# Performance work log

Hardware: AMD Instinct MI355X
Metric: run time of the kernel (lower is better)

## Reference

```python
import jax, jax.numpy as jnp
import numpy as np

B = 16          # graphs per batch
NPER = 1024     # nodes per graph (max_nodes for to_dense_batch)
N = B * NPER    # total nodes
D = 128         # hidden_dim
H = 8           # nhead
E = 524288      # total edges (avg degree 32)
DFF = 512       # dim_feedforward
LN_EPS = 1e-5


def setup_inputs() -> dict:
    key = jax.random.key(0)
    ks = jax.random.split(key, 26)
    w = lambda k, shape, s=0.05: (jax.random.normal(k, shape, jnp.float32) * s)
    h = jax.random.normal(ks[0], (N, D), jnp.float32)
    edge_index = jax.random.randint(ks[1], (2, E), 0, N, jnp.int32)
    edge_attr = jax.random.normal(ks[2], (E, D), jnp.float32)
    # nodes are in a random 'original' order; sort_idx sorts them by graph id
    sort_idx = jax.random.permutation(ks[3], N).astype(jnp.int32)
    unsort_idx = jnp.argsort(sort_idx).astype(jnp.int32)
    sorted_batch = jnp.repeat(jnp.arange(B, dtype=jnp.int32), NPER)
    batch = jnp.zeros((N,), jnp.int32).at[sort_idx].set(sorted_batch)
    return {
        "h": h, "edge_attr": edge_attr,
        # GINEConv: edge linear + 2-layer gin MLP
        "edge_w": w(ks[4], (D, D)), "edge_b": w(ks[5], (D,)),
        "gin_w1": w(ks[6], (D, D)), "gin_b1": w(ks[7], (D,)),
        "gin_w2": w(ks[8], (D, D)), "gin_b2": w(ks[9], (D,)),
        # MultiheadAttention packed qkv + out proj
        "in_proj_w": w(ks[10], (3 * D, D)), "in_proj_b": w(ks[11], (3 * D,)),
        "out_w": w(ks[12], (D, D)), "out_b": w(ks[13], (D,)),
        # FFN
        "ffn_w1": w(ks[14], (DFF, D)), "ffn_b1": w(ks[15], (DFF,)),
        "ffn_w2": w(ks[16], (D, DFF)), "ffn_b2": w(ks[17], (D,)),
        # LayerNorms
        "ln1_w": jnp.ones((D,)), "ln1_b": jnp.zeros((D,)),
        "ln2_w": jnp.ones((D,)), "ln2_b": jnp.zeros((D,)),
        "ln3_w": jnp.ones((D,)), "ln3_b": jnp.zeros((D,)),
        "edge_index": edge_index, "batch": batch,
        "sort_idx": sort_idx, "unsort_idx": unsort_idx,
    }


def _layer_norm(x, w, b):
    mu = x.mean(-1, keepdims=True)
    var = ((x - mu) ** 2).mean(-1, keepdims=True)
    return (x - mu) * jax.lax.rsqrt(var + LN_EPS) * w + b


def reference(h, edge_attr, edge_w, edge_b, gin_w1, gin_b1, gin_w2, gin_b2,
              in_proj_w, in_proj_b, out_w, out_b,
              ffn_w1, ffn_b1, ffn_w2, ffn_b2,
              ln1_w, ln1_b, ln2_w, ln2_b, ln3_w, ln3_b,
              edge_index, batch, sort_idx, unsort_idx):
    residual = h
    # ---- local branch: GINEConv (eps=0) -----------------------------------
    src, dst = edge_index[0], edge_index[1]
    e = edge_attr @ edge_w.T + edge_b                      # [E, D]
    msg = jax.nn.relu(h[src] + e)                          # gather + fuse
    agg = jax.ops.segment_sum(msg, dst, num_segments=N)    # scatter-add
    x = h + agg                                            # (1+eps)*x_i + aggr
    h_local = jax.nn.relu(x @ gin_w1.T + gin_b1) @ gin_w2.T + gin_b2
    # ---- global branch: sort -> dense batch -> MHA -> unsort --------------
    hs = h[sort_idx]
    bs = batch[sort_idx]
    counts = jax.ops.segment_sum(jnp.ones((N,), jnp.int32), bs, num_segments=B)
    ptr = jnp.concatenate([jnp.zeros((1,), jnp.int32),
                           jnp.cumsum(counts)[:-1].astype(jnp.int32)])
    pos = jnp.arange(N, dtype=jnp.int32) - ptr[bs]         # slot within graph
    dense = jnp.zeros((B, NPER, D), h.dtype).at[bs, pos].set(hs)
    mask = jnp.zeros((B, NPER), bool).at[bs, pos].set(True)
    qkv = dense @ in_proj_w.T + in_proj_b                  # [B, NPER, 3D]
    q, k, v = jnp.split(qkv, 3, axis=-1)
    hd = D // H
    q = q.reshape(B, NPER, H, hd)
    k = k.reshape(B, NPER, H, hd)
    v = v.reshape(B, NPER, H, hd)
    scores = jnp.einsum('bqhd,bkhd->bhqk', q, k) / np.float32(np.sqrt(hd))
    scores = jnp.where(mask[:, None, None, :], scores, jnp.float32(-1e9))
    attn = jax.nn.softmax(scores, axis=-1)
    ao = jnp.einsum('bhqk,bkhd->bqhd', attn, v).reshape(B, NPER, D)
    ao = ao @ out_w.T + out_b
    h_attn = ao[bs, pos][unsort_idx]                       # dense->flat->unsort
    # ---- residual + norms + FFN -------------------------------------------
    h1 = _layer_norm(residual + h_local, ln1_w, ln1_b)
    h2 = _layer_norm(h1 + h_attn, ln2_w, ln2_b)
    ffn = jax.nn.gelu(h2 @ ffn_w1.T + ffn_b1, approximate=False) @ ffn_w2.T + ffn_b2
    return _layer_norm(h2 + ffn, ln3_w, ln3_b)
```

## Files before the change

### kernel.cpp

```cpp
#include <hip/hip_runtime.h>
#include <cmath>

typedef __attribute__((ext_vector_type(4))) float  f32x4;
typedef __attribute__((ext_vector_type(16))) float f32x16;
typedef __attribute__((ext_vector_type(2))) float  f32x2;
typedef __attribute__((ext_vector_type(8))) short  s16x8;
typedef __attribute__((ext_vector_type(4))) short  s16x4;
typedef __attribute__((ext_vector_type(2))) short  s16x2;
typedef __attribute__((ext_vector_type(4))) int    i32x4;

#define DEV __device__ __forceinline__

DEV float bf2f(short s) {
    unsigned int u = ((unsigned int)(unsigned short)s) << 16;
    return __builtin_bit_cast(float, u);
}
DEV short f2bs(float f) {
    unsigned int x = __builtin_bit_cast(unsigned int, f);
    x += 0x7fffu + ((x >> 16) & 1u);
    return (short)(x >> 16);
}
DEV s16x8 ld8(const void* p, size_t off, int m) {
    s16x8 r;
    if (m) {
        const float* f = (const float*)p + off;
        f32x4 a = *(const f32x4*)f, b = *(const f32x4*)(f + 4);
#pragma unroll
        for (int j = 0; j < 4; ++j) { r[j] = f2bs(a[j]); r[4 + j] = f2bs(b[j]); }
    } else {
        r = *(const s16x8*)((const short*)p + off);
    }
    return r;
}
DEV float ldf(const void* p, size_t off, int m) {
    return m ? ((const float*)p)[off] : bf2f(((const short*)p)[off]);
}

__global__ void probe_kernel(const unsigned* __restrict__ w1, int* __restrict__ flag)
{
    if (threadIdx.x == 0 && blockIdx.x == 0)
        flag[0] = (w1[0] == 0x3F800000u) ? 1 : 0;
}

__global__ void hist_kernel(const int* __restrict__ edst, int* __restrict__ cnt)
{
    int e = blockIdx.x * 256 + threadIdx.x;
    atomicAdd(&cnt[edst[e]], 1);
}

__global__ __launch_bounds__(1024)
void scan_kernel(const int* __restrict__ cnt, int* __restrict__ cursor)
{
    __shared__ int s[1024];
    int t = threadIdx.x;
    int v[16];
    int sum = 0;
#pragma unroll
    for (int j = 0; j < 16; ++j) { v[j] = cnt[t * 16 + j]; sum += v[j]; }
    s[t] = sum;
    __syncthreads();
    for (int off = 1; off < 1024; off <<= 1) {
        int x = (t >= off) ? s[t - off] : 0;
        __syncthreads();
        s[t] += x;
        __syncthreads();
    }
    int running = s[t] - sum;
#pragma unroll
    for (int j = 0; j < 16; ++j) { cursor[t * 16 + j] = running; running += v[j]; }
}

__global__ void scatter_kernel(const int* __restrict__ esrc, const int* __restrict__ edst,
                               int* __restrict__ cursor, int* __restrict__ sEid,
                               int* __restrict__ sDst, int* __restrict__ sSrc)
{
    int e = blockIdx.x * 256 + threadIdx.x;
    int d = edst[e];
    int pos = atomicAdd(&cursor[d], 1);
    sEid[pos] = e;
    sDst[pos] = d;
    sSrc[pos] = esrc[e];
}

__global__ __launch_bounds__(256, 2)
void edge_agg_kernel(const void* __restrict__ EA, const void* __restrict__ EW,
                     const void* __restrict__ EB, const void* __restrict__ H,
                     const int* __restrict__ sEid, const int* __restrict__ sDst,
                     const int* __restrict__ sSrc,
                     float* __restrict__ agg, const int* __restrict__ modep)
{
    const int m = *modep;
    __shared__ short Ws[128][136];
    int tid = threadIdx.x;
#pragma unroll
    for (int i = 0; i < 8; ++i) {
        int id = i * 256 + tid;
        int r = id >> 4, c = (id & 15) << 3;
        *(s16x8*)&Ws[r][c] = ld8(EW, (size_t)r * 128 + c, m);
    }
    __syncthreads();

    int wave = tid >> 6, lane = tid & 63;
    int lq = lane & 15, quad = lane >> 4;
    int ebw = blockIdx.x * 256 + wave * 64;

    float ebias[8];
#pragma unroll
    for (int nt = 0; nt < 8; ++nt) ebias[nt] = ldf(EB, nt * 16 + lq, m);

    float run[8] = {};
    int run_d = -1;

    for (int t = 0; t < 4; ++t) {
        int arow = ebw + ((lq >> 2) << 4) + t * 4 + (lq & 3);
        int aeid = sEid[arow];
        s16x8 af[4];
        const size_t abase = (size_t)aeid * 128 + quad * 8;
#pragma unroll
        for (int kb = 0; kb < 4; ++kb)
            af[kb] = ld8(EA, abase + kb * 32, m);

        f32x4 acc[8] = {};
#pragma unroll
        for (int kb = 0; kb < 4; ++kb) {
#pragma unroll
            for (int nt = 0; nt < 8; ++nt) {
                s16x8 bfr = *(const s16x8*)&Ws[nt * 16 + lq][kb * 32 + quad * 8];
                acc[nt] = __builtin_amdgcn_mfma_f32_16x16x32_bf16(af[kb], bfr, acc[nt], 0, 0, 0);
            }
        }

        int pbase = ebw + quad * 16 + t * 4;
        i32x4 dv = *(const i32x4*)&sDst[pbase];
        i32x4 sv = *(const i32x4*)&sSrc[pbase];
#pragma unroll
        for (int r = 0; r < 4; ++r) {
            int d = dv[r];
            if (d != run_d) {
                if (run_d >= 0) {
#pragma unroll
                    for (int nt = 0; nt < 8; ++nt)
                        atomicAdd(&agg[(size_t)run_d * 128 + nt * 16 + lq], run[nt]);
                }
                run_d = d;
#pragma unroll
                for (int nt = 0; nt < 8; ++nt) run[nt] = 0.f;
            }
#pragma unroll
            for (int nt = 0; nt < 8; ++nt) {
                float v = acc[nt][r] + ebias[nt] + ldf(H, (size_t)sv[r] * 128 + nt * 16 + lq, m);
                run[nt] += fmaxf(v, 0.f);
            }
        }
    }
    if (run_d >= 0) {
#pragma unroll
        for (int nt = 0; nt < 8; ++nt)
            atomicAdd(&agg[(size_t)run_d * 128 + nt * 16 + lq], run[nt]);
    }
}

__global__ void xadd_kernel(const void* __restrict__ H, const float* __restrict__ agg,
                            short* __restrict__ X, const int* __restrict__ modep)
{
    const int m = *modep;
    int i = (blockIdx.x * 256 + threadIdx.x) * 4;
    float hv[4];
    if (m) { f32x4 t = *(const f32x4*)((const float*)H + i);
#pragma unroll
             for (int j = 0; j < 4; ++j) hv[j] = t[j]; }
    else   { s16x4 t = *(const s16x4*)((const short*)H + i);
#pragma unroll
             for (int j = 0; j < 4; ++j) hv[j] = bf2f(t[j]); }
    f32x4 av = *(const f32x4*)&agg[i];
    s16x4 o;
#pragma unroll
    for (int j = 0; j < 4; ++j) o[j] = f2bs(hv[j] + av[j]);
    *(s16x4*)&X[i] = o;
}

template<int KTOT, int ACT, bool GATHER, bool XIN>
__global__ __launch_bounds__(256, 2)
void gemm_bt(const void* __restrict__ X, const int* __restrict__ ridx,
             const void* __restrict__ W, const void* __restrict__ B,
             short* __restrict__ Y, int N, const int* __restrict__ modep)
{
    const int m = *modep;
    const int xm = XIN ? m : 0;
    __shared__ short As[64][136];
    __shared__ short Wsh[64][136];
    int tid = threadIdx.x;
    int wave = tid >> 6, lane = tid & 63;
    int lq = lane & 15, quad = lane >> 4;
    int mbase = blockIdx.x * 64, nbase = blockIdx.y * 64;

    f32x4 acc[4] = {};
    for (int kc = 0; kc < KTOT / 128; ++kc) {
#pragma unroll
        for (int i = 0; i < 4; ++i) {
            int id = i * 256 + tid;
            int r = id >> 4, c = (id & 15) << 3;
            int srow = GATHER ? ridx[mbase + r] : (mbase + r);
            *(s16x8*)&As[r][c]  = ld8(X, (size_t)srow * KTOT + kc * 128 + c, xm);
            *(s16x8*)&Wsh[r][c] = ld8(W, (size_t)(nbase + r) * KTOT + kc * 128 + c, m);
        }
        __syncthreads();
        s16x8 af[4];
#pragma unroll
        for (int kb = 0; kb < 4; ++kb)
            af[kb] = *(const s16x8*)&As[wave * 16 + lq][kb * 32 + quad * 8];
#pragma unroll
        for (int kb = 0; kb < 4; ++kb) {
#pragma unroll
            for (int nt = 0; nt < 4; ++nt) {
                s16x8 bfr = *(const s16x8*)&Wsh[nt * 16 + lq][kb * 32 + quad * 8];
                acc[nt] = __builtin_amdgcn_mfma_f32_16x16x32_bf16(af[kb], bfr, acc[nt], 0, 0, 0);
            }
        }
        __syncthreads();
    }
#pragma unroll
    for (int nt = 0; nt < 4; ++nt) {
        int col = nbase + nt * 16 + lq;
        float bias = ldf(B, col, m);
#pragma unroll
        for (int r = 0; r < 4; ++r) {
            int row = mbase + wave * 16 + quad * 4 + r;
            float v = acc[nt][r] + bias;
            if (ACT == 1) v = fmaxf(v, 0.f);
            if (ACT == 2) v = 0.5f * v * (1.f + erff(v * 0.70710678118f));
            Y[(size_t)row * N + col] = f2bs(v);
        }
    }
}

__global__ __launch_bounds__(256, 2)
void attn_kernel(const short* __restrict__ QKV, short* __restrict__ AO)
{
    __shared__ __align__(16) short Ks[2048][8];
    __shared__ __align__(16) short Vt[16][1032];
    int bid = blockIdx.x;
    int qc = bid & 3, bh = bid >> 2;
    int b = bh >> 3, hh = bh & 7;
    int t = threadIdx.x;
    const short* base = QKV + (size_t)b * 1024 * 384 + hh * 16;

#pragma unroll
    for (int i = 0; i < 8; ++i) {
        int idx = i * 256 + t;
        int c = idx >> 10, kv = idx & 1023;
        const short* r = base + (size_t)kv * 384;
        *(s16x8*)&Ks[c * 1024 + kv][0] = *(const s16x8*)&r[128 + c * 8];
        s16x8 v = *(const s16x8*)&r[256 + c * 8];
#pragma unroll
        for (int j = 0; j < 8; ++j) Vt[c * 8 + j][kv] = v[j];
    }
    __syncthreads();

    int wave = t >> 6, lane = t & 63;
    int ln = lane & 31, hi = lane >> 5;

    for (int t2 = 0; t2 < 2; ++t2) {
        int qrow = qc * 256 + t2 * 128 + wave * 32 + ln;
        s16x8 qf = *(const s16x8*)(base + (size_t)qrow * 384 + hi * 8);
        f32x16 oacc = {};
        f32x16 zacc = {};
        float den = 0.f;
        for (int kv0 = 0; kv0 < 1024; kv0 += 32) {
            s16x8 kf = *(const s16x8*)&Ks[hi * 1024 + kv0 + ln][0];
            f32x16 st = __builtin_amdgcn_mfma_f32_32x32x16_bf16(kf, qf, zacc, 0, 0, 0);
            float e[16];
#pragma unroll
            for (int r2 = 0; r2 < 16; ++r2) {
                e[r2] = __expf(fminf(st[r2] * 0.25f, 30.f));
                den += e[r2];
            }
            unsigned pw[8];
#pragma unroll
            for (int r2 = 0; r2 < 8; ++r2)
                pw[r2] = (unsigned)(unsigned short)f2bs(e[2 * r2])
                       | ((unsigned)(unsigned short)f2bs(e[2 * r2 + 1]) << 16);
            auto sA = __builtin_amdgcn_permlane32_swap((int)pw[0], (int)pw[2], false, false);
            auto sB = __builtin_amdgcn_permlane32_swap((int)pw[1], (int)pw[3], false, false);
            auto sC = __builtin_amdgcn_permlane32_swap((int)pw[4], (int)pw[6], false, false);
            auto sD = __builtin_amdgcn_permlane32_swap((int)pw[5], (int)pw[7], false, false);
            i32x4 f1 = { (int)sA[0], (int)sB[0], (int)sA[1], (int)sB[1] };
            i32x4 f2 = { (int)sC[0], (int)sD[0], (int)sC[1], (int)sD[1] };
            s16x8 vf1 = *(const s16x8*)&Vt[ln & 15][kv0 + hi * 8];
            s16x8 vf2 = *(const s16x8*)&Vt[ln & 15][kv0 + 16 + hi * 8];
            oacc = __builtin_amdgcn_mfma_f32_32x32x16_bf16(vf1, __builtin_bit_cast(s16x8, f1), oacc, 0, 0, 0);
            oacc = __builtin_amdgcn_mfma_f32_32x32x16_bf16(vf2, __builtin_bit_cast(s16x8, f2), oacc, 0, 0, 0);
        }
        den += __shfl_xor(den, 32);
        float inv = 1.f / den;
        short* orow = AO + (size_t)(b * 1024 + qrow) * 128 + hh * 16;
        s16x4 oA, oB;
#pragma unroll
        for (int r2 = 0; r2 < 4; ++r2) {
            oA[r2] = f2bs(oacc[r2] * inv);
            oB[r2] = f2bs(oacc[4 + r2] * inv);
        }
        *(s16x4*)&orow[hi * 4]     = oA;
        *(s16x4*)&orow[8 + hi * 4] = oB;
    }
}

template<bool AIN, bool FINAL>
__global__ __launch_bounds__(256)
void ln_kernel(const void* __restrict__ A, const short* __restrict__ Badd,
               const int* __restrict__ gidx,
               const void* __restrict__ w, const void* __restrict__ bb,
               void* __restrict__ outp, const int* __restrict__ modep)
{
    const int m = *modep;
    int wave = threadIdx.x >> 6, lane = threadIdx.x & 63;
    int row = blockIdx.x * 4 + wave;
    int grow = gidx ? gidx[row] : row;
    int c = lane * 2;
    float a0, a1;
    if (AIN && m) {
        f32x2 t = *(const f32x2*)&((const float*)A)[(size_t)row * 128 + c];
        a0 = t[0]; a1 = t[1];
    } else {
        s16x2 t = *(const s16x2*)&((const short*)A)[(size_t)row * 128 + c];
        a0 = bf2f(t[0]); a1 = bf2f(t[1]);
    }
    s16x2 bv = *(const s16x2*)&Badd[(size_t)grow * 128 + c];
    float x0 = a0 + bf2f(bv[0]);
    float x1 = a1 + bf2f(bv[1]);
    float s = x0 + x1;
#pragma unroll
    for (int o = 1; o < 64; o <<= 1) s += __shfl_xor(s, o);
    float mu = s * (1.f / 128.f);
    float d0 = x0 - mu, d1 = x1 - mu;
    float q = d0 * d0 + d1 * d1;
#pragma unroll
    for (int o = 1; o < 64; o <<= 1) q += __shfl_xor(q, o);
    float rs = rsqrtf(q * (1.f / 128.f) + 1e-5f);
    float y0 = d0 * rs * ldf(w, c, m)     + ldf(bb, c, m);
    float y1 = d1 * rs * ldf(w, c + 1, m) + ldf(bb, c + 1, m);
    if (FINAL && m) {
        f32x2 ov = {y0, y1};
        *(f32x2*)&((float*)outp)[(size_t)row * 128 + c] = ov;
    } else {
        s16x2 ov = {f2bs(y0), f2bs(y1)};
        *(s16x2*)&((short*)outp)[(size_t)row * 128 + c] = ov;
    }
}

extern "C" void kernel_launch(void* const* d_in, const int* in_sizes, int n_in,
                              void* d_out, int out_size, void* d_ws, size_t ws_size,
                              hipStream_t stream)
{
    const void* h   = d_in[0];
    const void* ea  = d_in[1];
    const void* edw = d_in[2];
    const void* edb = d_in[3];
    const void* gw1 = d_in[4];
    const void* gb1 = d_in[5];
    const void* gw2 = d_in[6];
    const void* gb2 = d_in[7];
    const void* ipw = d_in[8];
    const void* ipb = d_in[9];
    const void* ow  = d_in[10];
    const void* ob  = d_in[11];
    const void* fw1 = d_in[12];
    const void* fb1 = d_in[13];
    const void* fw2 = d_in[14];
    const void* fb2 = d_in[15];
    const void* l1w = d_in[16];
    const void* l1b = d_in[17];
    const void* l2w = d_in[18];
    const void* l2b = d_in[19];
    const void* l3w = d_in[20];
    const void* l3b = d_in[21];
    const int* ei    = (const int*)d_in[22];
    const int* sidx  = (const int*)d_in[24];
    const int* uidx  = (const int*)d_in[25];

    const int NN = 16384, EE = 524288;
    const size_t MB = 1024 * 1024;
    char* ws = (char*)d_ws;
    float* agg   = (float*)ws;
    short* mid   = (short*)(ws + 8 * MB);
    short* h1    = (short*)(ws + 12 * MB);
    short* qkv   = (short*)ws;
    short* atns  = (short*)(ws + 16 * MB);
    short* ffmid = (short*)ws;
    short* ffout = (short*)(ws + 16 * MB);
    short* h2    = (short*)(ws + 20 * MB);
    int*   flag  = (int*)(ws + 24 * MB);
    int* cnt    = (int*)(ws + 8 * MB);
    int* cursor = (int*)(ws + 8 * MB + 65536);
    int* sEid   = (int*)(ws + 9 * MB);
    int* sDst   = (int*)(ws + 11 * MB);
    int* sSrc   = (int*)(ws + 13 * MB);
    short* xbuf  = (short*)d_out;
    short* hloc  = (short*)d_out;
    short* ao    = (short*)d_out;

    probe_kernel<<<1, 64, 0, stream>>>((const unsigned*)l1w, flag);
    hipMemsetAsync(agg, 0, (size_t)NN * 128 * sizeof(float), stream);
    hipMemsetAsync(cnt, 0, (size_t)NN * sizeof(int), stream);
    hist_kernel<<<EE / 256, 256, 0, stream>>>(ei + EE, cnt);
    scan_kernel<<<1, 1024, 0, stream>>>(cnt, cursor);
    scatter_kernel<<<EE / 256, 256, 0, stream>>>(ei, ei + EE, cursor, sEid, sDst, sSrc);
    edge_agg_kernel<<<EE / 256, 256, 0, stream>>>(ea, edw, edb, h, sEid, sDst, sSrc, agg, flag);
    xadd_kernel<<<NN * 128 / 1024, 256, 0, stream>>>(h, agg, xbuf, flag);
    gemm_bt<128, 1, false, false><<<dim3(NN / 64, 2), 256, 0, stream>>>(xbuf, nullptr, gw1, gb1, mid, 128, flag);
    gemm_bt<128, 0, false, false><<<dim3(NN / 64, 2), 256, 0, stream>>>(mid, nullptr, gw2, gb2, hloc, 128, flag);
    ln_kernel<true, false><<<NN / 4, 256, 0, stream>>>(h, hloc, nullptr, l1w, l1b, h1, flag);
    gemm_bt<128, 0, true, true><<<dim3(NN / 64, 6), 256, 0, stream>>>(h, sidx, ipw, ipb, qkv, 384, flag);
    attn_kernel<<<512, 256, 0, stream>>>(qkv, ao);
    gemm_bt<128, 0, false, false><<<dim3(NN / 64, 2), 256, 0, stream>>>(ao, nullptr, ow, ob, atns, 128, flag);
    ln_kernel<false, false><<<NN / 4, 256, 0, stream>>>(h1, atns, uidx, l2w, l2b, h2, flag);
    gemm_bt<128, 2, false, false><<<dim3(NN / 64, 8), 256, 0, stream>>>(h2, nullptr, fw1, fb1, ffmid, 512, flag);
    gemm_bt<512, 0, false, false><<<dim3(NN / 64, 2), 256, 0, stream>>>(ffmid, nullptr, fw2, fb2, ffout, 128, flag);
    ln_kernel<false, true><<<NN / 4, 256, 0, stream>>>(h2, ffout, nullptr, l3w, l3b, d_out, flag);
}
```

Baseline: 716.8 us.

## Fuse GIN MLP with residual add and FFN with final LayerNorm

Replaces the xadd kernel and the two GIN GEMMs with one kernel that builds h+agg in shared memory and runs both 128x128 GEMMs back to back per 64-row tile. Likewise fuses FFN up-projection with GELU, down-projection, residual and the final LayerNorm into one kernel, keeping the 512-wide intermediate in LDS. This removes several global round trips and launches. The cost is large shared-memory use in the FFN kernel (about 100KB, one block per CU), only 256 blocks, and redundant per-block weight loads. The generic GEMM launch bound is also raised to 4 blocks per CU.

```diff
diff --git a/kernel.cpp b/kernel.cpp
--- a/kernel.cpp
+++ b/kernel.cpp
@@ -160,27 +160,224 @@
     }
 }
 
-__global__ void xadd_kernel(const void* __restrict__ H, const float* __restrict__ agg,
-                            short* __restrict__ X, const int* __restrict__ modep)
+__global__ __launch_bounds__(256, 2)
+void gin_fused_kernel(const void* __restrict__ H, const float* __restrict__ agg,
+                      const void* __restrict__ W1, const void* __restrict__ B1,
+                      const void* __restrict__ W2, const void* __restrict__ B2,
+                      short* __restrict__ Y, const int* __restrict__ modep)
 {
     const int m = *modep;
-    int i = (blockIdx.x * 256 + threadIdx.x) * 4;
-    float hv[4];
-    if (m) { f32x4 t = *(const f32x4*)((const float*)H + i);
-#pragma unroll
-             for (int j = 0; j < 4; ++j) hv[j] = t[j]; }
-    else   { s16x4 t = *(const s16x4*)((const short*)H + i);
-#pragma unroll
-             for (int j = 0; j < 4; ++j) hv[j] = bf2f(t[j]); }
-    f32x4 av = *(const f32x4*)&agg[i];
-    s16x4 o;
-#pragma unroll
-    for (int j = 0; j < 4; ++j) o[j] = f2bs(hv[j] + av[j]);
-    *(s16x4*)&X[i] = o;
+    __shared__ short As[64][136];
+    __shared__ short Wsh[128][136];
+    int tid = threadIdx.x;
+    int mbase = blockIdx.x * 64;
+
+#pragma unroll
+    for (int i = 0; i < 4; ++i) {
+        int id = i * 256 + tid;
+        int r = id >> 4, c = (id & 15) << 3;
+        size_t off = (size_t)(mbase + r) * 128 + c;
+        f32x4 a0 = *(const f32x4*)&agg[off];
+        f32x4 a1 = *(const f32x4*)&agg[off + 4];
+        s16x8 o;
+        if (m) {
+            const float* hf = (const float*)H + off;
+            f32x4 h0 = *(const f32x4*)hf, h1v = *(const f32x4*)(hf + 4);
+#pragma unroll
+            for (int j = 0; j < 4; ++j) { o[j] = f2bs(h0[j] + a0[j]); o[4 + j] = f2bs(h1v[j] + a1[j]); }
+        } else {
+            s16x8 hv = *(const s16x8*)((const short*)H + off);
+#pragma unroll
+            for (int j = 0; j < 4; ++j) { o[j] = f2bs(bf2f(hv[j]) + a0[j]); o[4 + j] = f2bs(bf2f(hv[4 + j]) + a1[j]); }
+        }
+        *(s16x8*)&As[r][c] = o;
+    }
+#pragma unroll
+    for (int i = 0; i < 8; ++i) {
+        int id = i * 256 + tid;
+        int r = id >> 4, c = (id & 15) << 3;
+        *(s16x8*)&Wsh[r][c] = ld8(W1, (size_t)r * 128 + c, m);
+    }
+    __syncthreads();
+
+    int wave = tid >> 6, lane = tid & 63;
+    int lq = lane & 15, quad = lane >> 4;
+
+    s16x8 af[4];
+#pragma unroll
+    for (int kb = 0; kb < 4; ++kb)
+        af[kb] = *(const s16x8*)&As[wave * 16 + lq][kb * 32 + quad * 8];
+    f32x4 acc[8] = {};
+#pragma unroll
+    for (int kb = 0; kb < 4; ++kb) {
+#pragma unroll
+        for (int nt = 0; nt < 8; ++nt) {
+            s16x8 bfr = *(const s16x8*)&Wsh[nt * 16 + lq][kb * 32 + quad * 8];
+            acc[nt] = __builtin_amdgcn_mfma_f32_16x16x32_bf16(af[kb], bfr, acc[nt], 0, 0, 0);
+        }
+    }
+#pragma unroll
+    for (int nt = 0; nt < 8; ++nt) {
+        float b = ldf(B1, nt * 16 + lq, m);
+#pragma unroll
+        for (int r = 0; r < 4; ++r)
+            As[wave * 16 + quad * 4 + r][nt * 16 + lq] = f2bs(fmaxf(acc[nt][r] + b, 0.f));
+    }
+    __syncthreads();
+#pragma unroll
+    for (int i = 0; i < 8; ++i) {
+        int id = i * 256 + tid;
+        int r = id >> 4, c = (id & 15) << 3;
+        *(s16x8*)&Wsh[r][c] = ld8(W2, (size_t)r * 128 + c, m);
+    }
+    __syncthreads();
+
+    s16x8 af2[4];
+#pragma unroll
+    for (int kb = 0; kb < 4; ++kb)
+        af2[kb] = *(const s16x8*)&As[wave * 16 + lq][kb * 32 + quad * 8];
+    f32x4 acc2[8] = {};
+#pragma unroll
+    for (int kb = 0; kb < 4; ++kb) {
+#pragma unroll
+        for (int nt = 0; nt < 8; ++nt) {
+            s16x8 bfr = *(const s16x8*)&Wsh[nt * 16 + lq][kb * 32 + quad * 8];
+            acc2[nt] = __builtin_amdgcn_mfma_f32_16x16x32_bf16(af2[kb], bfr, acc2[nt], 0, 0, 0);
+        }
+    }
+#pragma unroll
+    for (int nt = 0; nt < 8; ++nt) {
+        float b = ldf(B2, nt * 16 + lq, m);
+#pragma unroll
+        for (int r = 0; r < 4; ++r) {
+            int row = mbase + wave * 16 + quad * 4 + r;
+            Y[(size_t)row * 128 + nt * 16 + lq] = f2bs(acc2[nt][r] + b);
+        }
+    }
+}
+
+__global__ __launch_bounds__(256, 1)
+void ffn_fused_kernel(const short* __restrict__ X,
+                      const void* __restrict__ W1, const void* __restrict__ B1,
+                      const void* __restrict__ W2, const void* __restrict__ B2,
+                      const void* __restrict__ LW, const void* __restrict__ LB,
+                      void* __restrict__ outp, const int* __restrict__ modep)
+{
+    const int m = *modep;
+    __shared__ short As[64][136];
+    __shared__ short Wsh[128][136];
+    __shared__ short Mid[64][536];
+    int tid = threadIdx.x;
+    int mbase = blockIdx.x * 64;
+
+#pragma unroll
+    for (int i = 0; i < 4; ++i) {
+        int id = i * 256 + tid;
+        int r = id >> 4, c = (id & 15) << 3;
+        *(s16x8*)&As[r][c] = *(const s16x8*)&X[(size_t)(mbase + r) * 128 + c];
+    }
+
+    int wave = tid >> 6, lane = tid & 63;
+    int lq = lane & 15, quad = lane >> 4;
+
+    for (int cc = 0; cc < 4; ++cc) {
+#pragma unroll
+        for (int i = 0; i < 8; ++i) {
+            int id = i * 256 + tid;
+            int r = id >> 4, c = (id & 15) << 3;
+            *(s16x8*)&Wsh[r][c] = ld8(W1, (size_t)(cc * 128 + r) * 128 + c, m);
+        }
+        __syncthreads();
+        s16x8 af[4];
+#pragma unroll
+        for (int kb = 0; kb < 4; ++kb)
+            af[kb] = *(const s16x8*)&As[wave * 16 + lq][kb * 32 + quad * 8];
+        f32x4 acc[8] = {};
+#pragma unroll
+        for (int kb = 0; kb < 4; ++kb) {
+#pragma unroll
+            for (int nt = 0; nt < 8; ++nt) {
+                s16x8 bfr = *(const s16x8*)&Wsh[nt * 16 + lq][kb * 32 + quad * 8];
+                acc[nt] = __builtin_amdgcn_mfma_f32_16x16x32_bf16(af[kb], bfr, acc[nt], 0, 0, 0);
+            }
+        }
+#pragma unroll
+        for (int nt = 0; nt < 8; ++nt) {
+            float b = ldf(B1, cc * 128 + nt * 16 + lq, m);
+#pragma unroll
+            for (int r = 0; r < 4; ++r) {
+                float v = acc[nt][r] + b;
+                v = 0.5f * v * (1.f + erff(v * 0.70710678118f));
+                Mid[wave * 16 + quad * 4 + r][cc * 128 + nt * 16 + lq] = f2bs(v);
+            }
+        }
+        __syncthreads();
+    }
+
+    f32x4 acc2[8] = {};
+    for (int kc = 0; kc < 4; ++kc) {
+#pragma unroll
+        for (int i = 0; i < 8; ++i) {
+            int id = i * 256 + tid;
+            int r = id >> 4, c = (id & 15) << 3;
+            *(s16x8*)&Wsh[r][c] = ld8(W2, (size_t)r * 512 + kc * 128 + c, m);
+        }
+        __syncthreads();
+        s16x8 af2[4];
+#pragma unroll
+        for (int kb = 0; kb < 4; ++kb)
+            af2[kb] = *(const s16x8*)&Mid[wave * 16 + lq][kc * 128 + kb * 32 + quad * 8];
+#pragma unroll
+        for (int kb = 0; kb < 4; ++kb) {
+#pragma unroll
+            for (int nt = 0; nt < 8; ++nt) {
+                s16x8 bfr = *(const s16x8*)&Wsh[nt * 16 + lq][kb * 32 + quad * 8];
+                acc2[nt] = __builtin_amdgcn_mfma_f32_16x16x32_bf16(af2[kb], bfr, acc2[nt], 0, 0, 0);
+            }
+        }
+        __syncthreads();
+    }
+
+    float bb2[8], w3[8], b3[8];
+#pragma unroll
+    for (int nt = 0; nt < 8; ++nt) {
+        int col = nt * 16 + lq;
+        bb2[nt] = ldf(B2, col, m);
+        w3[nt]  = ldf(LW, col, m);
+        b3[nt]  = ldf(LB, col, m);
+    }
+#pragma unroll
+    for (int r = 0; r < 4; ++r) {
+        int lrow = wave * 16 + quad * 4 + r;
+        float x[8];
+        float s = 0.f;
+#pragma unroll
+        for (int nt = 0; nt < 8; ++nt) {
+            x[nt] = bf2f(As[lrow][nt * 16 + lq]) + acc2[nt][r] + bb2[nt];
+            s += x[nt];
+        }
+#pragma unroll
+        for (int o = 1; o < 16; o <<= 1) s += __shfl_xor(s, o);
+        float mu = s * (1.f / 128.f);
+        float q = 0.f;
+#pragma unroll
+        for (int nt = 0; nt < 8; ++nt) { float d = x[nt] - mu; q += d * d; }
+#pragma unroll
+        for (int o = 1; o < 16; o <<= 1) q += __shfl_xor(q, o);
+        float rs = rsqrtf(q * (1.f / 128.f) + 1e-5f);
+        size_t orow = (size_t)(mbase + lrow) * 128;
+#pragma unroll
+        for (int nt = 0; nt < 8; ++nt) {
+            int col = nt * 16 + lq;
+            float y = (x[nt] - mu) * rs * w3[nt] + b3[nt];
+            if (m) ((float*)outp)[orow + col] = y;
+            else   ((short*)outp)[orow + col] = f2bs(y);
+        }
+    }
 }
 
 template<int KTOT, int ACT, bool GATHER, bool XIN>
-__global__ __launch_bounds__(256, 2)
+__global__ __launch_bounds__(256, 4)
 void gemm_bt(const void* __restrict__ X, const int* __restrict__ ridx,
              const void* __restrict__ W, const void* __restrict__ B,
              short* __restrict__ Y, int N, const int* __restrict__ modep)
@@ -382,12 +579,9 @@
     const size_t MB = 1024 * 1024;
     char* ws = (char*)d_ws;
     float* agg   = (float*)ws;
-    short* mid   = (short*)(ws + 8 * MB);
+    short* qkv   = (short*)ws;
     short* h1    = (short*)(ws + 12 * MB);
-    short* qkv   = (short*)ws;
     short* atns  = (short*)(ws + 16 * MB);
-    short* ffmid = (short*)ws;
-    short* ffout = (short*)(ws + 16 * MB);
     short* h2    = (short*)(ws + 20 * MB);
     int*   flag  = (int*)(ws + 24 * MB);
     int* cnt    = (int*)(ws + 8 * MB);
@@ -395,7 +589,6 @@
     int* sEid   = (int*)(ws + 9 * MB);
     int* sDst   = (int*)(ws + 11 * MB);
     int* sSrc   = (int*)(ws + 13 * MB);
-    short* xbuf  = (short*)d_out;
     short* hloc  = (short*)d_out;
     short* ao    = (short*)d_out;
 
@@ -406,15 +599,11 @@
     scan_kernel<<<1, 1024, 0, stream>>>(cnt, cursor);
     scatter_kernel<<<EE / 256, 256, 0, stream>>>(ei, ei + EE, cursor, sEid, sDst, sSrc);
     edge_agg_kernel<<<EE / 256, 256, 0, stream>>>(ea, edw, edb, h, sEid, sDst, sSrc, agg, flag);
-    xadd_kernel<<<NN * 128 / 1024, 256, 0, stream>>>(h, agg, xbuf, flag);
-    gemm_bt<128, 1, false, false><<<dim3(NN / 64, 2), 256, 0, stream>>>(xbuf, nullptr, gw1, gb1, mid, 128, flag);
-    gemm_bt<128, 0, false, false><<<dim3(NN / 64, 2), 256, 0, stream>>>(mid, nullptr, gw2, gb2, hloc, 128, flag);
+    gin_fused_kernel<<<NN / 64, 256, 0, stream>>>(h, agg, gw1, gb1, gw2, gb2, hloc, flag);
     ln_kernel<true, false><<<NN / 4, 256, 0, stream>>>(h, hloc, nullptr, l1w, l1b, h1, flag);
     gemm_bt<128, 0, true, true><<<dim3(NN / 64, 6), 256, 0, stream>>>(h, sidx, ipw, ipb, qkv, 384, flag);
     attn_kernel<<<512, 256, 0, stream>>>(qkv, ao);
     gemm_bt<128, 0, false, false><<<dim3(NN / 64, 2), 256, 0, stream>>>(ao, nullptr, ow, ob, atns, 128, flag);
     ln_kernel<false, false><<<NN / 4, 256, 0, stream>>>(h1, atns, uidx, l2w, l2b, h2, flag);
-    gemm_bt<128, 2, false, false><<<dim3(NN / 64, 8), 256, 0, stream>>>(h2, nullptr, fw1, fb1, ffmid, 512, flag);
-    gemm_bt<512, 0, false, false><<<dim3(NN / 64, 2), 256, 0, stream>>>(ffmid, nullptr, fw2, fb2, ffout, 128, flag);
-    ln_kernel<false, true><<<NN / 4, 256, 0, stream>>>(h2, ffout, nullptr, l3w, l3b, d_out, flag);
-}
+    ffn_fused_kernel<<<NN / 64, 256, 0, stream>>>(h2, fw1, fb1, fw2, fb2, l3w, l3b, d_out, flag);
+}
```

New measurement: 725.8 us. Within noise of the previous version (+1.3%).
